# Kernel optimization log

Hardware: AMD Instinct MI355X
Metric: run time of the kernel (lower is better)

The kernel has to match this reference:

```python
import math
import jax, jax.numpy as jnp
import numpy as np

HEADS = 16
REL_WINDOW = 128


def setup_inputs() -> dict:
    key = jax.random.key(0)
    k1, k2, k3, k4, k5 = jax.random.split(key, 5)
    b, s, d = 2, 2048, 1024
    hd = d // HEADS          # 64
    R = 2 * REL_WINDOW + 1   # 257
    return {
        "x": jax.random.normal(k1, (b, s, d), dtype=jnp.float32),
        "Wqkv": jax.random.normal(k2, (3 * d, d), dtype=jnp.float32) * (1.0 / math.sqrt(d)),
        "bqkv": jax.random.normal(k3, (3 * d,), dtype=jnp.float32) * 0.02,
        "Wr": jax.random.normal(k4, (R, hd), dtype=jnp.float32) * (1.0 / math.sqrt(hd)),
        "br": jax.random.normal(k5, (R,), dtype=jnp.float32) * 0.02,
    }


def reference(x, Wqkv, bqkv, Wr, br):
    b, s, d = x.shape
    h = HEADS
    hd = d // h
    w = REL_WINDOW
    scale = math.sqrt(d / h)

    # qkv projection; torch view(b,s,h,3*hd) then chunk(3, dim=-1)
    qkv = (x @ Wqkv.T + bqkv).reshape(b, s, h, 3 * hd)
    q, k, v = jnp.split(qkv, 3, axis=-1)          # each [b,s,h,hd]
    q = q.transpose(0, 2, 1, 3)                   # [b,h,s,hd]
    k = k.transpose(0, 2, 1, 3)
    v = v.transpose(0, 2, 1, 3)

    # content scores
    content = jnp.einsum('bhik,bhjk->bhij', q, k) / scale  # [b,h,s,s]

    # relative position scores: project queries to R logits, gather per (i,j) offset
    idx = jnp.arange(s)
    offsets = jnp.clip(idx[None, :] - idx[:, None], -w, w) + w  # [s,s] in [0, 2w]
    rp = jnp.einsum('bhik,rk->bhir', q, Wr) + br               # [b,h,s,R]
    pos = jnp.take_along_axis(rp, jnp.broadcast_to(offsets, (b, h, s, s)), axis=-1)

    attn = jax.nn.softmax(content + pos, axis=-1)
    out = jnp.einsum('bhij,bhjk->bhik', attn, v)  # [b,h,s,hd]
    return out.transpose(0, 2, 1, 3).reshape(b, s, d)
```

## Files before the change

kernel.cpp:

```cpp
#include <hip/hip_runtime.h>

typedef short bfrag __attribute__((ext_vector_type(8)));
typedef float f32x4 __attribute__((ext_vector_type(4)));

#define MFMA16(a, b, c) __builtin_amdgcn_mfma_f32_16x16x32_bf16((a), (b), (c), 0, 0, 0)

#define SEQ   2048
#define DMOD  1024
#define NHEAD 16
#define HDIM  64
#define RSZ   257
#define RPADN 272
#define XN    (4096*1024)
#define WN    (3072*1024)
#define LOG2E 1.44269504f

__device__ __forceinline__ unsigned short f2bf(float f) {
  unsigned int u = __float_as_uint(f);
  u += 0x7FFFu + ((u >> 16) & 1u);
  return (unsigned short)(u >> 16);
}
__device__ __forceinline__ float bf2f(unsigned short u) {
  return __uint_as_float(((unsigned int)u) << 16);
}
__device__ __forceinline__ unsigned int pkbf(float a, float b) {
#if defined(__gfx950__)
  unsigned int r;
  asm("v_cvt_pk_bf16_f32 %0, %1, %2" : "=v"(r) : "v"(a), "v"(b));
  return r;
#else
  return (unsigned int)f2bf(a) | ((unsigned int)f2bf(b) << 16);
#endif
}
__device__ __forceinline__ float fexp2(float x) {
#if __has_builtin(__builtin_amdgcn_exp2f)
  return __builtin_amdgcn_exp2f(x);
#else
  return __expf(x * 0.69314718f);
#endif
}
__device__ __forceinline__ void gl2lds16(const void* g, void* l) {
  __builtin_amdgcn_global_load_lds(
      (__attribute__((address_space(1))) void*)(g),
      (__attribute__((address_space(3))) void*)(l), 16, 0, 0);
}

__global__ __launch_bounds__(256) void cast_all(const float* __restrict__ x,
                                                const float* __restrict__ Wqkv,
                                                const float* __restrict__ Wr,
                                                unsigned short* __restrict__ xb,
                                                unsigned short* __restrict__ wb,
                                                unsigned short* __restrict__ wrb) {
  int i = (blockIdx.x * 256 + threadIdx.x) * 4;
  if (i < XN) {
    float4 v = *(const float4*)(x + i);
    ushort4 o; o.x = f2bf(v.x); o.y = f2bf(v.y); o.z = f2bf(v.z); o.w = f2bf(v.w);
    *(ushort4*)(xb + i) = o;
  } else if (i < XN + WN) {
    int j = i - XN;
    float4 v = *(const float4*)(Wqkv + j);
    ushort4 o; o.x = f2bf(v.x); o.y = f2bf(v.y); o.z = f2bf(v.z); o.w = f2bf(v.w);
    *(ushort4*)(wb + j) = o;
  } else {
    int j = i - XN - WN;
    ushort4 o;
    unsigned short t[4];
#pragma unroll
    for (int k = 0; k < 4; ++k)
      t[k] = (j + k < RSZ * HDIM) ? f2bf(Wr[j + k]) : (unsigned short)0;
    o.x = t[0]; o.y = t[1]; o.z = t[2]; o.w = t[3];
    *(ushort4*)(wrb + j) = o;
  }
}

__global__ __launch_bounds__(256) void qkv_gemm(const unsigned short* __restrict__ xb,
                                                const unsigned short* __restrict__ wb,
                                                const float* __restrict__ bqkv,
                                                unsigned short* __restrict__ qb,
                                                unsigned short* __restrict__ kbuf,
                                                unsigned short* __restrict__ vb) {
  __shared__ unsigned short As[128 * 64];
  __shared__ unsigned short Bs[128 * 64];
  const int tid = threadIdx.x;
  const int m0 = blockIdx.y * 128, n0 = blockIdx.x * 128;
  const int wave = tid >> 6, lane = tid & 63;
  const int q4 = lane >> 4, l16 = lane & 15;
  const int wm = (wave & 1) * 64, wn = (wave >> 1) * 64;
  const int sw = l16 & 7;

  f32x4 acc[4][4];
#pragma unroll
  for (int rt = 0; rt < 4; ++rt)
#pragma unroll
    for (int ct = 0; ct < 4; ++ct) acc[rt][ct] = (f32x4){0.f, 0.f, 0.f, 0.f};

  for (int k0 = 0; k0 < DMOD; k0 += 64) {
#pragma unroll
    for (int it = 0; it < 4; ++it) {
      int ch = it * 256 + tid;
      int r = ch >> 3, cl = (ch & 7) ^ (r & 7);
      gl2lds16(xb + (size_t)(m0 + r) * DMOD + k0 + cl * 8, As + ch * 8);
      gl2lds16(wb + (size_t)(n0 + r) * DMOD + k0 + cl * 8, Bs + ch * 8);
    }
    __syncthreads();
#pragma unroll
    for (int ks = 0; ks < 2; ++ks) {
      bfrag af[4], bf[4];
#pragma unroll
      for (int rt = 0; rt < 4; ++rt)
        af[rt] = *(const bfrag*)(As + (wm + rt * 16 + l16) * 64 + ((ks * 4 + q4) ^ sw) * 8);
#pragma unroll
      for (int ct = 0; ct < 4; ++ct)
        bf[ct] = *(const bfrag*)(Bs + (wn + ct * 16 + l16) * 64 + ((ks * 4 + q4) ^ sw) * 8);
#pragma unroll
      for (int rt = 0; rt < 4; ++rt)
#pragma unroll
        for (int ct = 0; ct < 4; ++ct)
          acc[rt][ct] = MFMA16(af[rt], bf[ct], acc[rt][ct]);
    }
    __syncthreads();
  }

#pragma unroll
  for (int rt = 0; rt < 4; ++rt) {
#pragma unroll
    for (int ct = 0; ct < 4; ++ct) {
      int n = n0 + wn + ct * 16 + l16;
      int hh = n / 192;
      int rem = n - hh * 192;
      int t = rem >> 6, dd = rem & 63;
      float bias = bqkv[n];
#pragma unroll
      for (int reg = 0; reg < 4; ++reg) {
        int m = m0 + wm + rt * 16 + q4 * 4 + reg;
        int bidx = m >> 11, sidx = m & 2047;
        unsigned short bv = f2bf(acc[rt][ct][reg] + bias);
        size_t hb = (size_t)(bidx * NHEAD + hh);
        size_t o = (hb * SEQ + sidx) * HDIM + dd;
        if (t == 0)      qb[o] = bv;
        else if (t == 1) kbuf[o] = bv;
        else             vb[o] = bv;
      }
    }
  }
}

__global__ __launch_bounds__(256) void vtrans(const unsigned short* __restrict__ vb,
                                              unsigned short* __restrict__ vtb) {
  __shared__ unsigned short T[64 * 80];
  const int tid = threadIdx.x;
  const int s0 = blockIdx.x * 64;
  const int bh = blockIdx.y;
  const unsigned short* src = vb + ((size_t)bh * SEQ + s0) * HDIM;
#pragma unroll
  for (int it = 0; it < 2; ++it) {
    int idx = it * 256 + tid;
    int r = idx >> 3, c = idx & 7;
    *(uint4*)(&T[r * 80 + c * 8]) = *(const uint4*)(src + r * HDIM + c * 8);
  }
  __syncthreads();
#pragma unroll
  for (int it = 0; it < 2; ++it) {
    int idx = it * 256 + tid;
    int d = idx >> 3, c = idx & 7;
    unsigned short tmp[8];
#pragma unroll
    for (int k = 0; k < 8; ++k) tmp[k] = T[(c * 8 + k) * 80 + d];
    *(uint4*)(vtb + ((size_t)bh * HDIM + d) * SEQ + s0 + c * 8) = *(uint4*)tmp;
  }
}

__global__ __launch_bounds__(256) void rp_gemm(const unsigned short* __restrict__ qb,
                                               const unsigned short* __restrict__ wrb,
                                               const float* __restrict__ br,
                                               unsigned short* __restrict__ rp16) {
  __shared__ unsigned short WrS[RPADN * HDIM];
  __shared__ unsigned short Qs[64 * HDIM];
  const int tid = threadIdx.x;
  const size_t row0 = (size_t)blockIdx.x * 64;

  for (int i = tid; i < RPADN * HDIM / 8; i += 256)
    *(uint4*)(&WrS[i * 8]) = *(const uint4*)(&wrb[i * 8]);
  for (int i = tid; i < 512; i += 256)
    *(uint4*)(&Qs[i * 8]) = *(const uint4*)(&qb[row0 * HDIM + i * 8]);
  __syncthreads();

  const int wave = tid >> 6, lane = tid & 63;
  const int q4 = lane >> 4, l16 = lane & 15;

  bfrag af0 = *(const bfrag*)(Qs + (wave * 16 + l16) * 64 + q4 * 8);
  bfrag af1 = *(const bfrag*)(Qs + (wave * 16 + l16) * 64 + 32 + q4 * 8);

#pragma unroll 4
  for (int ct = 0; ct < 17; ++ct) {
    f32x4 acc = (f32x4){0.f, 0.f, 0.f, 0.f};
    bfrag b0 = *(const bfrag*)(WrS + (ct * 16 + l16) * 64 + q4 * 8);
    bfrag b1 = *(const bfrag*)(WrS + (ct * 16 + l16) * 64 + 32 + q4 * 8);
    acc = MFMA16(af0, b0, acc);
    acc = MFMA16(af1, b1, acc);
    int col = ct * 16 + l16;
    if (col < RSZ) {
      float bias = br[col];
#pragma unroll
      for (int reg = 0; reg < 4; ++reg) {
        size_t rr = row0 + wave * 16 + q4 * 4 + reg;
        rp16[rr * RSZ + col] = f2bf((acc[reg] + bias) * LOG2E);
      }
    }
  }
}

__global__ __launch_bounds__(256) void flash_attn(const unsigned short* __restrict__ qb,
                                                  const unsigned short* __restrict__ kbuf,
                                                  const unsigned short* __restrict__ vtb,
                                                  const unsigned short* __restrict__ rp16,
                                                  float* __restrict__ out) {
  __shared__ unsigned short Ks[64 * 64];
  __shared__ unsigned short Vs[64 * 64];
  __shared__ unsigned short Ps[64 * 64];

  const int tid = threadIdx.x;
  const int i0 = blockIdx.x * 64;
  const int bh = blockIdx.y;
  const int wave = tid >> 6, lane = tid & 63;
  const int q4 = lane >> 4, l16 = lane & 15;
  const int sw = l16 & 7;
  const float SC = 0.125f * LOG2E;

  const int rloc = wave * 16 + l16;
  const int ig = i0 + rloc;
  const unsigned short* qrow = qb + ((size_t)bh * SEQ + ig) * HDIM;
  bfrag qf0 = *(const bfrag*)(qrow + q4 * 8);
  bfrag qf1 = *(const bfrag*)(qrow + 32 + q4 * 8);

  const unsigned short* rpbase = rp16 + ((size_t)bh * SEQ + ig) * RSZ;
  const float rpL = bf2f(rpbase[0]);
  const float rpR = bf2f(rpbase[256]);

  float m_s = -3.0e38f, l_s = 0.f;
  f32x4 oacc[4];
#pragma unroll
  for (int ct = 0; ct < 4; ++ct) oacc[ct] = (f32x4){0.f, 0.f, 0.f, 0.f};

  const unsigned short* kbase = kbuf + (size_t)bh * SEQ * HDIM;
  const unsigned short* vbase = vtb + (size_t)bh * HDIM * SEQ;

  for (int jt = 0; jt < 32; ++jt) {
    const int j0 = jt * 64;
#pragma unroll
    for (int it = 0; it < 2; ++it) {
      int ch = it * 256 + tid;
      int r = ch >> 3, cl = (ch & 7) ^ (r & 7);
      gl2lds16(kbase + (size_t)(j0 + r) * HDIM + cl * 8, Ks + ch * 8);
      gl2lds16(vbase + (size_t)r * SEQ + j0 + cl * 8, Vs + ch * 8);
    }
    __syncthreads();

    f32x4 sacc[4];
#pragma unroll
    for (int ct = 0; ct < 4; ++ct) {
      sacc[ct] = (f32x4){0.f, 0.f, 0.f, 0.f};
      bfrag k0f = *(const bfrag*)(Ks + (ct * 16 + l16) * 64 + (q4 ^ sw) * 8);
      bfrag k1f = *(const bfrag*)(Ks + (ct * 16 + l16) * 64 + ((4 + q4) ^ sw) * 8);
      sacc[ct] = MFMA16(k0f, qf0, sacc[ct]);
      sacc[ct] = MFMA16(k1f, qf1, sacc[ct]);
    }

    float p[4][4];
    const int dj = j0 - i0;
    if (dj >= 191) {
#pragma unroll
      for (int ct = 0; ct < 4; ++ct)
#pragma unroll
        for (int reg = 0; reg < 4; ++reg)
          p[ct][reg] = sacc[ct][reg] * SC + rpR;
    } else if (dj <= -191) {
#pragma unroll
      for (int ct = 0; ct < 4; ++ct)
#pragma unroll
        for (int reg = 0; reg < 4; ++reg)
          p[ct][reg] = sacc[ct][reg] * SC + rpL;
    } else {
#pragma unroll
      for (int ct = 0; ct < 4; ++ct) {
#pragma unroll
        for (int reg = 0; reg < 4; ++reg) {
          int j = j0 + ct * 16 + q4 * 4 + reg;
          int off = j - ig;
          off = (off < -128) ? -128 : (off > 128 ? 128 : off);
          p[ct][reg] = sacc[ct][reg] * SC + bf2f(rpbase[off + 128]);
        }
      }
    }

    float mm;
    {
      float a0 = fmaxf(fmaxf(p[0][0], p[0][1]), fmaxf(p[0][2], p[0][3]));
      float a1 = fmaxf(fmaxf(p[1][0], p[1][1]), fmaxf(p[1][2], p[1][3]));
      float a2 = fmaxf(fmaxf(p[2][0], p[2][1]), fmaxf(p[2][2], p[2][3]));
      float a3 = fmaxf(fmaxf(p[3][0], p[3][1]), fmaxf(p[3][2], p[3][3]));
      mm = fmaxf(fmaxf(a0, a1), fmaxf(a2, a3));
      mm = fmaxf(mm, __shfl_xor(mm, 16));
      mm = fmaxf(mm, __shfl_xor(mm, 32));
    }
    const float mnew = fmaxf(m_s, mm);
    const float alpha = fexp2(m_s - mnew);
    m_s = mnew;
#pragma unroll
    for (int ct = 0; ct < 4; ++ct)
#pragma unroll
      for (int reg = 0; reg < 4; ++reg)
        p[ct][reg] = fexp2(p[ct][reg] - m_s);
    {
      float s0 = (p[0][0] + p[0][1]) + (p[0][2] + p[0][3]);
      float s1 = (p[1][0] + p[1][1]) + (p[1][2] + p[1][3]);
      float s2 = (p[2][0] + p[2][1]) + (p[2][2] + p[2][3]);
      float s3 = (p[3][0] + p[3][1]) + (p[3][2] + p[3][3]);
      float rs = (s0 + s1) + (s2 + s3);
      rs += __shfl_xor(rs, 16);
      rs += __shfl_xor(rs, 32);
      l_s = l_s * alpha + rs;
    }
#pragma unroll
    for (int ct = 0; ct < 4; ++ct)
#pragma unroll
      for (int reg = 0; reg < 4; ++reg)
        oacc[ct][reg] *= alpha;

    unsigned int* Pw = (unsigned int*)Ps;
#pragma unroll
    for (int ct = 0; ct < 4; ++ct) {
      unsigned int pk01 = pkbf(p[ct][0], p[ct][1]);
      unsigned int pk23 = pkbf(p[ct][2], p[ct][3]);
      int jb = ct * 16 + q4 * 4;
      int chunk = jb >> 3;
      unsigned int a = rloc * 32 + ((chunk ^ sw) << 2) + ((q4 & 1) << 1);
      Pw[a] = pk01;
      Pw[a + 1] = pk23;
    }

    bfrag pf0 = *(const bfrag*)(Ps + rloc * 64 + (q4 ^ sw) * 8);
    bfrag pf1 = *(const bfrag*)(Ps + rloc * 64 + ((4 + q4) ^ sw) * 8);
#pragma unroll
    for (int ct = 0; ct < 4; ++ct) {
      bfrag v0f = *(const bfrag*)(Vs + (ct * 16 + l16) * 64 + (q4 ^ sw) * 8);
      bfrag v1f = *(const bfrag*)(Vs + (ct * 16 + l16) * 64 + ((4 + q4) ^ sw) * 8);
      oacc[ct] = MFMA16(v0f, pf0, oacc[ct]);
      oacc[ct] = MFMA16(v1f, pf1, oacc[ct]);
    }
    __syncthreads();
  }

  const int bidx = bh >> 4, hh = bh & 15;
  const float inv = 1.0f / l_s;
  float* orow = out + ((size_t)bidx * SEQ + ig) * DMOD + hh * HDIM;
#pragma unroll
  for (int ct = 0; ct < 4; ++ct) {
    float4 v;
    v.x = oacc[ct][0] * inv;
    v.y = oacc[ct][1] * inv;
    v.z = oacc[ct][2] * inv;
    v.w = oacc[ct][3] * inv;
    *(float4*)(orow + ct * 16 + q4 * 4) = v;
  }
}

extern "C" void kernel_launch(void* const* d_in, const int* in_sizes, int n_in,
                              void* d_out, int out_size, void* d_ws, size_t ws_size,
                              hipStream_t stream) {
  const float* x    = (const float*)d_in[0];
  const float* Wqkv = (const float*)d_in[1];
  const float* bqkv = (const float*)d_in[2];
  const float* Wr   = (const float*)d_in[3];
  const float* br   = (const float*)d_in[4];
  float* out = (float*)d_out;

  char* ws = (char*)d_ws;
  unsigned short* xb   = (unsigned short*)(ws);
  unsigned short* wb   = (unsigned short*)(ws + 8388608);
  unsigned short* qb   = (unsigned short*)(ws + 14680064);
  unsigned short* kb   = (unsigned short*)(ws + 23068672);
  unsigned short* vb   = (unsigned short*)(ws + 31457280);
  unsigned short* vtb  = (unsigned short*)(ws + 39845888);
  unsigned short* wrb  = (unsigned short*)(ws + 48234496);
  unsigned short* rp16 = (unsigned short*)(ws + 48269312);

  cast_all<<<7185, 256, 0, stream>>>(x, Wqkv, Wr, xb, wb, wrb);
  qkv_gemm<<<dim3(24, 32), 256, 0, stream>>>(xb, wb, bqkv, qb, kb, vb);
  vtrans<<<dim3(32, 32), 256, 0, stream>>>(vb, vtb);
  rp_gemm<<<1024, 256, 0, stream>>>(qb, wrb, br, rp16);
  flash_attn<<<dim3(32, 32), 256, 0, stream>>>(qb, kb, vtb, rp16, out);
}
```

Before: 237.7 us.

## Stage QKV epilogue through LDS for vector stores; widen attention KV tiles to 128

The QKV GEMM epilogue now writes bias-added bf16 results into swizzled shared memory, then stores 16-byte vectors to the Q/K/V head-major buffers instead of scattered 2-byte stores. The flash attention kernel loads 128-key K and V tiles per barrier pair and processes them as two 64-key halves, which halves the number of __syncthreads and global-to-LDS load phases. The cost is more LDS per block, which may reduce occupancy, plus an extra LDS round trip and barrier in the GEMM epilogue.

Measured after the change: 246.7 us. +3.8%, slower.

```diff
diff --git a/kernel.cpp b/kernel.cpp
--- a/kernel.cpp
+++ b/kernel.cpp
@@ -79,8 +79,9 @@
                                                 unsigned short* __restrict__ qb,
                                                 unsigned short* __restrict__ kbuf,
                                                 unsigned short* __restrict__ vb) {
-  __shared__ unsigned short As[128 * 64];
-  __shared__ unsigned short Bs[128 * 64];
+  __shared__ unsigned short SMEM[2 * 128 * 64];
+  unsigned short* As = SMEM;
+  unsigned short* Bs = SMEM + 128 * 64;
   const int tid = threadIdx.x;
   const int m0 = blockIdx.y * 128, n0 = blockIdx.x * 128;
   const int wave = tid >> 6, lane = tid & 63;
@@ -121,27 +122,37 @@
     __syncthreads();
   }
 
+  unsigned short* Cs = SMEM;
 #pragma unroll
   for (int rt = 0; rt < 4; ++rt) {
 #pragma unroll
     for (int ct = 0; ct < 4; ++ct) {
-      int n = n0 + wn + ct * 16 + l16;
-      int hh = n / 192;
-      int rem = n - hh * 192;
-      int t = rem >> 6, dd = rem & 63;
-      float bias = bqkv[n];
+      int n = wn + ct * 16 + l16;
+      float bias = bqkv[n0 + n];
+      int c = n >> 3, nl = n & 7;
 #pragma unroll
       for (int reg = 0; reg < 4; ++reg) {
-        int m = m0 + wm + rt * 16 + q4 * 4 + reg;
-        int bidx = m >> 11, sidx = m & 2047;
-        unsigned short bv = f2bf(acc[rt][ct][reg] + bias);
-        size_t hb = (size_t)(bidx * NHEAD + hh);
-        size_t o = (hb * SEQ + sidx) * HDIM + dd;
-        if (t == 0)      qb[o] = bv;
-        else if (t == 1) kbuf[o] = bv;
-        else             vb[o] = bv;
-      }
-    }
+        int m = wm + rt * 16 + q4 * 4 + reg;
+        int s = ((m >> 3) ^ m) & 7;
+        Cs[m * 128 + ((c ^ s) << 3) + nl] = f2bf(acc[rt][ct][reg] + bias);
+      }
+    }
+  }
+  __syncthreads();
+#pragma unroll
+  for (int it = 0; it < 8; ++it) {
+    int idx = it * 256 + tid;
+    int r = idx >> 4, c = idx & 15;
+    int s = ((r >> 3) ^ r) & 7;
+    bfrag val = *(const bfrag*)(Cs + r * 128 + (((c & 8) | ((c & 7) ^ s)) << 3));
+    int ng = n0 + c * 8;
+    int hh = ng / 192;
+    int rem = ng - hh * 192;
+    int t = rem >> 6, dd = rem & 63;
+    int mg = m0 + r;
+    size_t o = (((size_t)((mg >> 11) * NHEAD + hh)) * SEQ + (mg & 2047)) * HDIM + dd;
+    unsigned short* dst = (t == 0) ? qb : (t == 1) ? kbuf : vb;
+    *(bfrag*)(dst + o) = val;
   }
 }
 
@@ -215,8 +226,8 @@
                                                   const unsigned short* __restrict__ vtb,
                                                   const unsigned short* __restrict__ rp16,
                                                   float* __restrict__ out) {
-  __shared__ unsigned short Ks[64 * 64];
-  __shared__ unsigned short Vs[64 * 64];
+  __shared__ unsigned short Ks[128 * 64];
+  __shared__ unsigned short Vs[64 * 128];
   __shared__ unsigned short Ps[64 * 64];
 
   const int tid = threadIdx.x;
@@ -245,108 +256,121 @@
   const unsigned short* kbase = kbuf + (size_t)bh * SEQ * HDIM;
   const unsigned short* vbase = vtb + (size_t)bh * HDIM * SEQ;
 
-  for (int jt = 0; jt < 32; ++jt) {
-    const int j0 = jt * 64;
-#pragma unroll
-    for (int it = 0; it < 2; ++it) {
+  for (int jt = 0; jt < 16; ++jt) {
+    const int jb = jt * 128;
+#pragma unroll
+    for (int it = 0; it < 4; ++it) {
       int ch = it * 256 + tid;
-      int r = ch >> 3, cl = (ch & 7) ^ (r & 7);
-      gl2lds16(kbase + (size_t)(j0 + r) * HDIM + cl * 8, Ks + ch * 8);
-      gl2lds16(vbase + (size_t)r * SEQ + j0 + cl * 8, Vs + ch * 8);
+      int rk = ch >> 3, clk = (ch & 7) ^ (rk & 7);
+      gl2lds16(kbase + (size_t)(jb + rk) * HDIM + clk * 8, Ks + ch * 8);
+      int rv = ch >> 4, cv = ch & 15;
+      int clv = (cv & 8) | ((cv & 7) ^ (rv & 7));
+      gl2lds16(vbase + (size_t)rv * SEQ + jb + clv * 8, Vs + ch * 8);
     }
     __syncthreads();
 
-    f32x4 sacc[4];
-#pragma unroll
-    for (int ct = 0; ct < 4; ++ct) {
-      sacc[ct] = (f32x4){0.f, 0.f, 0.f, 0.f};
-      bfrag k0f = *(const bfrag*)(Ks + (ct * 16 + l16) * 64 + (q4 ^ sw) * 8);
-      bfrag k1f = *(const bfrag*)(Ks + (ct * 16 + l16) * 64 + ((4 + q4) ^ sw) * 8);
-      sacc[ct] = MFMA16(k0f, qf0, sacc[ct]);
-      sacc[ct] = MFMA16(k1f, qf1, sacc[ct]);
-    }
-
-    float p[4][4];
-    const int dj = j0 - i0;
-    if (dj >= 191) {
+#pragma unroll
+    for (int jh = 0; jh < 2; ++jh) {
+      const int j0 = jb + jh * 64;
+      const int jrb = jh * 64;
+
+      f32x4 sacc[4];
+#pragma unroll
+      for (int ct = 0; ct < 4; ++ct) {
+        sacc[ct] = (f32x4){0.f, 0.f, 0.f, 0.f};
+        const unsigned short* krow = Ks + (jrb + ct * 16 + l16) * 64;
+        bfrag k0f = *(const bfrag*)(krow + (q4 ^ sw) * 8);
+        bfrag k1f = *(const bfrag*)(krow + ((4 + q4) ^ sw) * 8);
+        sacc[ct] = MFMA16(k0f, qf0, sacc[ct]);
+        sacc[ct] = MFMA16(k1f, qf1, sacc[ct]);
+      }
+
+      float p[4][4];
+      const int dj = j0 - i0;
+      if (dj >= 191) {
+#pragma unroll
+        for (int ct = 0; ct < 4; ++ct)
+#pragma unroll
+          for (int reg = 0; reg < 4; ++reg)
+            p[ct][reg] = sacc[ct][reg] * SC + rpR;
+      } else if (dj <= -191) {
+#pragma unroll
+        for (int ct = 0; ct < 4; ++ct)
+#pragma unroll
+          for (int reg = 0; reg < 4; ++reg)
+            p[ct][reg] = sacc[ct][reg] * SC + rpL;
+      } else {
+#pragma unroll
+        for (int ct = 0; ct < 4; ++ct) {
+#pragma unroll
+          for (int reg = 0; reg < 4; ++reg) {
+            int j = j0 + ct * 16 + q4 * 4 + reg;
+            int off = j - ig;
+            off = (off < -128) ? -128 : (off > 128 ? 128 : off);
+            p[ct][reg] = sacc[ct][reg] * SC + bf2f(rpbase[off + 128]);
+          }
+        }
+      }
+
+      float mm;
+      {
+        float a0 = fmaxf(fmaxf(p[0][0], p[0][1]), fmaxf(p[0][2], p[0][3]));
+        float a1 = fmaxf(fmaxf(p[1][0], p[1][1]), fmaxf(p[1][2], p[1][3]));
+        float a2 = fmaxf(fmaxf(p[2][0], p[2][1]), fmaxf(p[2][2], p[2][3]));
+        float a3 = fmaxf(fmaxf(p[3][0], p[3][1]), fmaxf(p[3][2], p[3][3]));
+        mm = fmaxf(fmaxf(a0, a1), fmaxf(a2, a3));
+        mm = fmaxf(mm, __shfl_xor(mm, 16));
+        mm = fmaxf(mm, __shfl_xor(mm, 32));
+      }
+      const float mnew = fmaxf(m_s, mm);
+      const float alpha = fexp2(m_s - mnew);
+      m_s = mnew;
 #pragma unroll
       for (int ct = 0; ct < 4; ++ct)
 #pragma unroll
         for (int reg = 0; reg < 4; ++reg)
-          p[ct][reg] = sacc[ct][reg] * SC + rpR;
-    } else if (dj <= -191) {
+          p[ct][reg] = fexp2(p[ct][reg] - m_s);
+      {
+        float s0 = (p[0][0] + p[0][1]) + (p[0][2] + p[0][3]);
+        float s1 = (p[1][0] + p[1][1]) + (p[1][2] + p[1][3]);
+        float s2 = (p[2][0] + p[2][1]) + (p[2][2] + p[2][3]);
+        float s3 = (p[3][0] + p[3][1]) + (p[3][2] + p[3][3]);
+        float rs = (s0 + s1) + (s2 + s3);
+        rs += __shfl_xor(rs, 16);
+        rs += __shfl_xor(rs, 32);
+        l_s = l_s * alpha + rs;
+      }
 #pragma unroll
       for (int ct = 0; ct < 4; ++ct)
 #pragma unroll
         for (int reg = 0; reg < 4; ++reg)
-          p[ct][reg] = sacc[ct][reg] * SC + rpL;
-    } else {
+          oacc[ct][reg] *= alpha;
+
+      unsigned int* Pw = (unsigned int*)Ps;
 #pragma unroll
       for (int ct = 0; ct < 4; ++ct) {
-#pragma unroll
-        for (int reg = 0; reg < 4; ++reg) {
-          int j = j0 + ct * 16 + q4 * 4 + reg;
-          int off = j - ig;
-          off = (off < -128) ? -128 : (off > 128 ? 128 : off);
-          p[ct][reg] = sacc[ct][reg] * SC + bf2f(rpbase[off + 128]);
-        }
-      }
-    }
-
-    float mm;
-    {
-      float a0 = fmaxf(fmaxf(p[0][0], p[0][1]), fmaxf(p[0][2], p[0][3]));
-      float a1 = fmaxf(fmaxf(p[1][0], p[1][1]), fmaxf(p[1][2], p[1][3]));
-      float a2 = fmaxf(fmaxf(p[2][0], p[2][1]), fmaxf(p[2][2], p[2][3]));
-      float a3 = fmaxf(fmaxf(p[3][0], p[3][1]), fmaxf(p[3][2], p[3][3]));
-      mm = fmaxf(fmaxf(a0, a1), fmaxf(a2, a3));
-      mm = fmaxf(mm, __shfl_xor(mm, 16));
-      mm = fmaxf(mm, __shfl_xor(mm, 32));
-    }
-    const float mnew = fmaxf(m_s, mm);
-    const float alpha = fexp2(m_s - mnew);
-    m_s = mnew;
-#pragma unroll
-    for (int ct = 0; ct < 4; ++ct)
-#pragma unroll
-      for (int reg = 0; reg < 4; ++reg)
-        p[ct][reg] = fexp2(p[ct][reg] - m_s);
-    {
-      float s0 = (p[0][0] + p[0][1]) + (p[0][2] + p[0][3]);
-      float s1 = (p[1][0] + p[1][1]) + (p[1][2] + p[1][3]);
-      float s2 = (p[2][0] + p[2][1]) + (p[2][2] + p[2][3]);
-      float s3 = (p[3][0] + p[3][1]) + (p[3][2] + p[3][3]);
-      float rs = (s0 + s1) + (s2 + s3);
-      rs += __shfl_xor(rs, 16);
-      rs += __shfl_xor(rs, 32);
-      l_s = l_s * alpha + rs;
-    }
-#pragma unroll
-    for (int ct = 0; ct < 4; ++ct)
-#pragma unroll
-      for (int reg = 0; reg < 4; ++reg)
-        oacc[ct][reg] *= alpha;
-
-    unsigned int* Pw = (unsigned int*)Ps;
-#pragma unroll
-    for (int ct = 0; ct < 4; ++ct) {
-      unsigned int pk01 = pkbf(p[ct][0], p[ct][1]);
-      unsigned int pk23 = pkbf(p[ct][2], p[ct][3]);
-      int jb = ct * 16 + q4 * 4;
-      int chunk = jb >> 3;
-      unsigned int a = rloc * 32 + ((chunk ^ sw) << 2) + ((q4 & 1) << 1);
-      Pw[a] = pk01;
-      Pw[a + 1] = pk23;
-    }
-
-    bfrag pf0 = *(const bfrag*)(Ps + rloc * 64 + (q4 ^ sw) * 8);
-    bfrag pf1 = *(const bfrag*)(Ps + rloc * 64 + ((4 + q4) ^ sw) * 8);
-#pragma unroll
-    for (int ct = 0; ct < 4; ++ct) {
-      bfrag v0f = *(const bfrag*)(Vs + (ct * 16 + l16) * 64 + (q4 ^ sw) * 8);
-      bfrag v1f = *(const bfrag*)(Vs + (ct * 16 + l16) * 64 + ((4 + q4) ^ sw) * 8);
-      oacc[ct] = MFMA16(v0f, pf0, oacc[ct]);
-      oacc[ct] = MFMA16(v1f, pf1, oacc[ct]);
+        unsigned int pk01 = pkbf(p[ct][0], p[ct][1]);
+        unsigned int pk23 = pkbf(p[ct][2], p[ct][3]);
+        int chunk = ct * 2 + (q4 >> 1);
+        unsigned int a = rloc * 32 + ((chunk ^ sw) << 2) + ((q4 & 1) << 1);
+        Pw[a] = pk01;
+        Pw[a + 1] = pk23;
+      }
+
+      bfrag pf0 = *(const bfrag*)(Ps + rloc * 64 + (q4 ^ sw) * 8);
+      bfrag pf1 = *(const bfrag*)(Ps + rloc * 64 + ((4 + q4) ^ sw) * 8);
+      const int c0 = jh * 8 + q4;
+      const int c1 = jh * 8 + 4 + q4;
+      const int p0 = (c0 & 8) | ((c0 & 7) ^ sw);
+      const int p1 = (c1 & 8) | ((c1 & 7) ^ sw);
+#pragma unroll
+      for (int ct = 0; ct < 4; ++ct) {
+        const unsigned short* vrow = Vs + (ct * 16 + l16) * 128;
+        bfrag v0f = *(const bfrag*)(vrow + p0 * 8);
+        bfrag v1f = *(const bfrag*)(vrow + p1 * 8);
+        oacc[ct] = MFMA16(v0f, pf0, oacc[ct]);
+        oacc[ct] = MFMA16(v1f, pf1, oacc[ct]);
+      }
     }
     __syncthreads();
   }
```

## Fuse V transpose into QKV GEMM epilogue via shared-memory staged stores

Applied to the files above, without the earlier changes.

The QKV GEMM epilogue now stages the bf16 output tile in swizzled shared memory, then writes Q and K with 16-byte vector stores and writes V directly in transposed layout. This removes the separate vtrans kernel launch and its extra round trip of V through global memory, and replaces the scattered 2-byte scalar stores. It adds a synchronisation and shared-memory transpose work to the GEMM tail. A small index simplification in flash_attn is cosmetic.

After: 232.4 us. 1.02x faster.

```diff
diff --git a/kernel.cpp b/kernel.cpp
--- a/kernel.cpp
+++ b/kernel.cpp
@@ -78,9 +78,10 @@
                                                 const float* __restrict__ bqkv,
                                                 unsigned short* __restrict__ qb,
                                                 unsigned short* __restrict__ kbuf,
-                                                unsigned short* __restrict__ vb) {
-  __shared__ unsigned short As[128 * 64];
-  __shared__ unsigned short Bs[128 * 64];
+                                                unsigned short* __restrict__ vtb) {
+  __shared__ unsigned short SMEM[2 * 128 * 64];
+  unsigned short* As = SMEM;
+  unsigned short* Bs = SMEM + 128 * 64;
   const int tid = threadIdx.x;
   const int m0 = blockIdx.y * 128, n0 = blockIdx.x * 128;
   const int wave = tid >> 6, lane = tid & 63;
@@ -121,52 +122,65 @@
     __syncthreads();
   }
 
+  unsigned short* Cs = SMEM;
 #pragma unroll
   for (int rt = 0; rt < 4; ++rt) {
 #pragma unroll
     for (int ct = 0; ct < 4; ++ct) {
-      int n = n0 + wn + ct * 16 + l16;
-      int hh = n / 192;
-      int rem = n - hh * 192;
-      int t = rem >> 6, dd = rem & 63;
-      float bias = bqkv[n];
+      int n = wn + ct * 16 + l16;
+      float bias = bqkv[n0 + n];
+      int c = n >> 3, nl = n & 7;
 #pragma unroll
       for (int reg = 0; reg < 4; ++reg) {
-        int m = m0 + wm + rt * 16 + q4 * 4 + reg;
-        int bidx = m >> 11, sidx = m & 2047;
-        unsigned short bv = f2bf(acc[rt][ct][reg] + bias);
-        size_t hb = (size_t)(bidx * NHEAD + hh);
-        size_t o = (hb * SEQ + sidx) * HDIM + dd;
-        if (t == 0)      qb[o] = bv;
-        else if (t == 1) kbuf[o] = bv;
-        else             vb[o] = bv;
+        int m = wm + rt * 16 + q4 * 4 + reg;
+        int s = ((m >> 3) ^ m) & 7;
+        Cs[m * 128 + ((c ^ s) << 3) + nl] = f2bf(acc[rt][ct][reg] + bias);
       }
     }
   }
-}
-
-__global__ __launch_bounds__(256) void vtrans(const unsigned short* __restrict__ vb,
-                                              unsigned short* __restrict__ vtb) {
-  __shared__ unsigned short T[64 * 80];
-  const int tid = threadIdx.x;
-  const int s0 = blockIdx.x * 64;
-  const int bh = blockIdx.y;
-  const unsigned short* src = vb + ((size_t)bh * SEQ + s0) * HDIM;
-#pragma unroll
-  for (int it = 0; it < 2; ++it) {
+  __syncthreads();
+
+  const int batch = m0 >> 11;
+  const int sbase = m0 & 2047;
+  const int r3 = blockIdx.x % 3;
+  const bool hasV = (r3 != 0);
+  const int nv0 = n0 + ((r3 == 2) ? 64 : 0);
+
+#pragma unroll
+  for (int it = 0; it < 8; ++it) {
     int idx = it * 256 + tid;
-    int r = idx >> 3, c = idx & 7;
-    *(uint4*)(&T[r * 80 + c * 8]) = *(const uint4*)(src + r * HDIM + c * 8);
-  }
-  __syncthreads();
-#pragma unroll
-  for (int it = 0; it < 2; ++it) {
-    int idx = it * 256 + tid;
-    int d = idx >> 3, c = idx & 7;
-    unsigned short tmp[8];
-#pragma unroll
-    for (int k = 0; k < 8; ++k) tmp[k] = T[(c * 8 + k) * 80 + d];
-    *(uint4*)(vtb + ((size_t)bh * HDIM + d) * SEQ + s0 + c * 8) = *(uint4*)tmp;
+    int r = idx >> 4, c = idx & 15;
+    int ng = n0 + c * 8;
+    int hh = ng / 192;
+    int rem = ng - hh * 192;
+    int t = rem >> 6, dd = rem & 63;
+    if (t == 2) continue;
+    int s = ((r >> 3) ^ r) & 7;
+    bfrag val = *(const bfrag*)(Cs + r * 128 + (((c & 8) | ((c & 7) ^ s)) << 3));
+    size_t o = (((size_t)(batch * NHEAD + hh)) * SEQ + (sbase + r)) * HDIM + dd;
+    unsigned short* dst = (t == 0) ? qb : kbuf;
+    *(bfrag*)(dst + o) = val;
+  }
+
+  if (hasV) {
+    const int hh = nv0 / 192;
+    unsigned short* vdst = vtb + ((size_t)(batch * NHEAD + hh)) * HDIM * SEQ;
+    const int cbase = nv0 - n0;
+#pragma unroll
+    for (int it = 0; it < 4; ++it) {
+      int u = it * 256 + tid;
+      int dd = u >> 4, rc = u & 15;
+      int nloc = cbase + dd;
+      int c = nloc >> 3, nl = nloc & 7;
+      unsigned short tmp[8];
+#pragma unroll
+      for (int k = 0; k < 8; ++k) {
+        int m = rc * 8 + k;
+        int s = ((m >> 3) ^ m) & 7;
+        tmp[k] = Cs[m * 128 + (((c & 8) | ((c & 7) ^ s)) << 3) + nl];
+      }
+      *(uint4*)(vdst + (size_t)dd * SEQ + sbase + rc * 8) = *(uint4*)tmp;
+    }
   }
 }
 
@@ -332,8 +346,7 @@
     for (int ct = 0; ct < 4; ++ct) {
       unsigned int pk01 = pkbf(p[ct][0], p[ct][1]);
       unsigned int pk23 = pkbf(p[ct][2], p[ct][3]);
-      int jb = ct * 16 + q4 * 4;
-      int chunk = jb >> 3;
+      int chunk = ct * 2 + (q4 >> 1);
       unsigned int a = rloc * 32 + ((chunk ^ sw) << 2) + ((q4 & 1) << 1);
       Pw[a] = pk01;
       Pw[a + 1] = pk23;
@@ -380,14 +393,12 @@
   unsigned short* wb   = (unsigned short*)(ws + 8388608);
   unsigned short* qb   = (unsigned short*)(ws + 14680064);
   unsigned short* kb   = (unsigned short*)(ws + 23068672);
-  unsigned short* vb   = (unsigned short*)(ws + 31457280);
-  unsigned short* vtb  = (unsigned short*)(ws + 39845888);
-  unsigned short* wrb  = (unsigned short*)(ws + 48234496);
-  unsigned short* rp16 = (unsigned short*)(ws + 48269312);
+  unsigned short* vtb  = (unsigned short*)(ws + 31457280);
+  unsigned short* wrb  = (unsigned short*)(ws + 39845888);
+  unsigned short* rp16 = (unsigned short*)(ws + 39880704);
 
   cast_all<<<7185, 256, 0, stream>>>(x, Wqkv, Wr, xb, wb, wrb);
-  qkv_gemm<<<dim3(24, 32), 256, 0, stream>>>(xb, wb, bqkv, qb, kb, vb);
-  vtrans<<<dim3(32, 32), 256, 0, stream>>>(vb, vtb);
+  qkv_gemm<<<dim3(24, 32), 256, 0, stream>>>(xb, wb, bqkv, qb, kb, vtb);
   rp_gemm<<<1024, 256, 0, stream>>>(qb, wrb, br, rp16);
   flash_attn<<<dim3(32, 32), 256, 0, stream>>>(qb, kb, vtb, rp16, out);
 }
```
